# Optimization experiments

Hardware: AMD Instinct MI355X
Metric: run time of the kernel (lower is better)

The kernel has to match this reference:

```python
import jax, jax.numpy as jnp
import numpy as np

E4M3_MAX = 448.0  # max finite value of float8_e4m3fn
TILE = 64


def tile_quant_dequant(x):
    # per-row 1x64 tile quantization: scale = amax(tile)/448, fp8 e4m3 round-trip
    M, K = x.shape
    xt = x.reshape(M, K // TILE, TILE)
    amax = jnp.max(jnp.abs(xt), axis=-1, keepdims=True)
    scale = jnp.maximum(amax, 1e-12) / E4M3_MAX
    q = (xt / scale).astype(jnp.float8_e4m3fn).astype(jnp.float32)
    return (q * scale).reshape(M, K)


def block_quant_dequant(w):
    # 64x64 block quantization of the weight matrix
    N, K = w.shape
    wb = w.reshape(N // TILE, TILE, K // TILE, TILE)
    amax = jnp.max(jnp.abs(wb), axis=(1, 3), keepdims=True)
    scale = jnp.maximum(amax, 1e-12) / E4M3_MAX
    q = (wb / scale).astype(jnp.float8_e4m3fn).astype(jnp.float32)
    return (q * scale).reshape(N, K)


def setup_inputs() -> dict:
    key = jax.random.key(0)
    k1, k2 = jax.random.split(key)
    B, S, K, N = 2, 4096, 4096, 4096
    x = jax.random.normal(k1, (B, S, K), dtype=jnp.float32)
    # kaiming_uniform_(a=sqrt(5)) on [N,K] -> U(-1/sqrt(K), 1/sqrt(K))
    bound = float(1.0 / np.sqrt(K))
    weight = jax.random.uniform(k2, (N, K), jnp.float32, -bound, bound)
    bias = jnp.zeros((N,), jnp.float32)
    return {"x": x, "weight": weight, "bias": bias}


def reference(x, weight, bias):
    N, K = weight.shape
    x2d = x.reshape(-1, K)                     # [M, K]
    xq = tile_quant_dequant(x2d)               # simulated fp8 tile-quantized input
    wq = block_quant_dequant(weight)           # simulated fp8 block-quantized weight
    # fp8 GEMM with scales == matmul of dequantized operands (fp32 accumulation),
    # low-precision output then fp32 bias add (bf16 + fp32 bias -> fp32 in torch)
    out = jnp.matmul(xq, wq.T).astype(jnp.bfloat16).astype(jnp.float32)
    out = out + bias
    return out.reshape(*x.shape[:-1], N)
```

## Files before the change

kernel.cpp:

```cpp
#include <hip/hip_runtime.h>

typedef __attribute__((ext_vector_type(2))) float f32x2;
typedef __attribute__((ext_vector_type(4))) float f32x4;
typedef __attribute__((ext_vector_type(16))) float f32x16;
typedef __attribute__((ext_vector_type(4))) int i32x4;
typedef __attribute__((ext_vector_type(8))) int i32x8;

__device__ __forceinline__ unsigned char enc_e4m3(float y) {
    unsigned int u = __float_as_uint(y);
    unsigned int s = (u >> 31) << 7;
    unsigned int a = u & 0x7fffffffu;
    if (a >= 0x3C800000u) {
        unsigned int r = a + 0x7FFFFu + ((a >> 20) & 1u);
        r &= 0xFFF00000u;
        if (r > 0x43E00000u) r = 0x43E00000u;
        unsigned int e = (r >> 23) - 120u;
        return (unsigned char)(s | (e << 3) | ((r >> 20) & 7u));
    } else {
        int m = (int)rintf(__uint_as_float(a) * 512.0f);
        return (unsigned char)(s | (unsigned)m);
    }
}

__device__ __forceinline__ unsigned short f32_to_bf16_bits(float f) {
    unsigned int u = __float_as_uint(f);
    u += 0x7FFFu + ((u >> 16) & 1u);
    return (unsigned short)(u >> 16);
}

__global__ __launch_bounds__(256) void quant_x_kernel(const float* __restrict__ x,
                                                      unsigned char* __restrict__ xq,
                                                      float* __restrict__ xsT,
                                                      long long n4, int K, int M) {
    long long g = (long long)blockIdx.x * 256 + threadIdx.x;
    if (g >= n4) return;
    f32x4 v = ((const f32x4*)x)[g];
    float a = fmaxf(fmaxf(fabsf(v.x), fabsf(v.y)), fmaxf(fabsf(v.z), fabsf(v.w)));
    a = fmaxf(a, __shfl_xor(a, 1));
    a = fmaxf(a, __shfl_xor(a, 2));
    a = fmaxf(a, __shfl_xor(a, 4));
    a = fmaxf(a, __shfl_xor(a, 8));
    float scale = fmaxf(a, 1e-12f) / 448.0f;
    long long flat = g * 4;
    uchar4 o;
    o.x = enc_e4m3(v.x / scale);
    o.y = enc_e4m3(v.y / scale);
    o.z = enc_e4m3(v.z / scale);
    o.w = enc_e4m3(v.w / scale);
    *(uchar4*)(xq + flat) = o;
    int row = (int)(flat / K);
    int rem = (int)(flat % K);
    if ((rem & 63) == 0)
        xsT[(size_t)(rem >> 6) * M + row] = scale;
}

__global__ __launch_bounds__(256) void quant_w_kernel(const float* __restrict__ w,
                                                      unsigned char* __restrict__ wq,
                                                      float* __restrict__ ws,
                                                      int N, int K) {
    const int nb = blockIdx.y, kb = blockIdx.x;
    const int KT = K >> 6;
    const int t = threadIdx.x;
    const int rgrp = t >> 4;
    const int cchk = t & 15;
    f32x4 v[4];
    float a = 0.0f;
#pragma unroll
    for (int i = 0; i < 4; ++i) {
        int row = nb * 64 + rgrp + i * 16;
        v[i] = *(const f32x4*)(w + (size_t)row * K + kb * 64 + cchk * 4);
        a = fmaxf(a, fmaxf(fmaxf(fabsf(v[i].x), fabsf(v[i].y)),
                           fmaxf(fabsf(v[i].z), fabsf(v[i].w))));
    }
#pragma unroll
    for (int off = 1; off < 64; off <<= 1) a = fmaxf(a, __shfl_xor(a, off));
    __shared__ float sm[4];
    if ((t & 63) == 0) sm[t >> 6] = a;
    __syncthreads();
    a = fmaxf(fmaxf(sm[0], sm[1]), fmaxf(sm[2], sm[3]));
    float scale = fmaxf(a, 1e-12f) / 448.0f;
#pragma unroll
    for (int i = 0; i < 4; ++i) {
        int row = nb * 64 + rgrp + i * 16;
        uchar4 o;
        o.x = enc_e4m3(v[i].x / scale);
        o.y = enc_e4m3(v[i].y / scale);
        o.z = enc_e4m3(v[i].z / scale);
        o.w = enc_e4m3(v[i].w / scale);
        *(uchar4*)(wq + (size_t)row * K + kb * 64 + cchk * 4) = o;
    }
    if (t == 0) ws[(size_t)nb * KT + kb] = scale;
}

#define GLDS(srcp, ldsp) __builtin_amdgcn_global_load_lds( \
    (__attribute__((address_space(1))) void*)(srcp),       \
    (__attribute__((address_space(3))) void*)(ldsp), 16, 0, 0)

__global__ __launch_bounds__(512, 2) void gemm_fp8(const unsigned char* __restrict__ Aq,
                                                   const unsigned char* __restrict__ Bq,
                                                   const float* __restrict__ xsT,
                                                   const float* __restrict__ wss,
                                                   const float* __restrict__ bias,
                                                   float* __restrict__ C,
                                                   int M, int N, int K) {
    __shared__ unsigned char Al[32768];
    __shared__ unsigned char Bl[32768];
    __shared__ float xs_l[64 * 256];
    __shared__ float ws_l[4 * 64];
    const int tid = threadIdx.x;
    const int wid = tid >> 6;
    const int lane = tid & 63;
    const int wm = wid >> 2, wn = wid & 3;
    const int l31 = lane & 31, h = lane >> 5;
    const int KT = K >> 6, NT = KT;

    const int nbx = N >> 8;
    const int nwg = (M >> 8) * nbx;
    const int bid = blockIdx.x;
    const int swz = (bid & 7) * (nwg >> 3) + (bid >> 3);
    const int tm = swz / nbx, tn = swz % nbx;

    const unsigned char* gA = Aq + (size_t)tm * 256 * K;
    const unsigned char* gB = Bq + (size_t)tn * 256 * K;

    const int gswz = (((lane & 3) ^ ((lane >> 3) & 3)) << 4);

    const int fsw = (l31 >> 1) & 3;
    const int slotLo = (2 * h) ^ fsw;
    const int oX = (wm * 128 + l31) * 64;
    const int oW = (wn * 64 + l31) * 64;
    const int oXlo = oX + slotLo * 16, oXhi = oX + (slotLo ^ 1) * 16;
    const int oWlo = oW + slotLo * 16, oWhi = oW + (slotLo ^ 1) * 16;

    const int xsoff = wm * 128 + l31;

    const f32x16 z16 = {0.f,0.f,0.f,0.f,0.f,0.f,0.f,0.f,0.f,0.f,0.f,0.f,0.f,0.f,0.f,0.f};
    f32x16 macc[2][4];
#pragma unroll
    for (int n = 0; n < 2; ++n)
#pragma unroll
        for (int m = 0; m < 4; ++m) macc[n][m] = z16;

    i32x8 xf[4], wf[2];
    float xsr[4], wsr = 0.f, scl[4];

    auto STG = [&](int t64, int bufn) {
#pragma unroll
        for (int i = 0; i < 2; ++i) {
            int seg = wid * 2 + i;
            int row = seg * 16 + (lane >> 2);
            size_t go = (size_t)row * K + (size_t)t64 * 64 + gswz;
            GLDS(gA + go, (char*)Al + bufn * 16384 + seg * 1024);
            GLDS(gB + go, (char*)Bl + bufn * 16384 + seg * 1024);
        }
    };

    auto RD_S = [&](int t) {
#pragma unroll
        for (int m = 0; m < 4; ++m) xsr[m] = xs_l[t * 256 + xsoff + m * 32];
        wsr = ws_l[wn * KT + t];
    };

    auto RD_X = [&](const unsigned char* p, int mi) {
        ((i32x4*)&xf[mi])[0] = *(const i32x4*)(p + oXlo + mi * 2048);
        ((i32x4*)&xf[mi])[1] = *(const i32x4*)(p + oXhi + mi * 2048);
    };
    auto RD_W = [&](const unsigned char* p, int ni) {
        ((i32x4*)&wf[ni])[0] = *(const i32x4*)(p + oWlo + ni * 2048);
        ((i32x4*)&wf[ni])[1] = *(const i32x4*)(p + oWhi + ni * 2048);
    };

    auto RD_ALL = [&](const unsigned char* pXp, const unsigned char* pWp) {
        RD_W(pWp, 0); RD_W(pWp, 1);
        RD_X(pXp, 0); RD_X(pXp, 1); RD_X(pXp, 2); RD_X(pXp, 3);
    };

    auto RESC = [&](f32x16& acc, const f32x16& p, float s) {
        f32x2 sv = {s, s};
#pragma unroll
        for (int k = 0; k < 8; ++k) {
            f32x2 a = {acc[2 * k], acc[2 * k + 1]};
            f32x2 q = {p[2 * k], p[2 * k + 1]};
            a = __builtin_elementwise_fma(q, sv, a);
            acc[2 * k] = a.x;
            acc[2 * k + 1] = a.y;
        }
    };

    auto CL = [&](int ni, int mi0) {
#pragma unroll
        for (int q = 0; q < 2; ++q) {
            const int mi = mi0 + q;
            f32x16 p = __builtin_amdgcn_mfma_scale_f32_32x32x64_f8f6f4(
                wf[ni], xf[mi], z16, 0, 0, 0, 0x7F7F7F7F, 0, 0x7F7F7F7F);
            RESC(macc[ni][mi], p, scl[mi]);
        }
    };

    const int xtot = KT * 256;
    for (int idx = tid; idx < xtot; idx += 512)
        xs_l[idx] = xsT[(size_t)(idx >> 8) * M + tm * 256 + (idx & 255)];
    for (int idx = tid; idx < 4 * KT; idx += 512)
        ws_l[idx] = wss[(size_t)(tn * 4 + idx / KT) * KT + (idx % KT)];
    STG(0, 0);
    __syncthreads();
    RD_S(0);
    RD_ALL(Al, Bl);

    for (int t = 0; t < NT; ++t) {
        const int buf = t & 1;
        const unsigned char* pXn = Al + (buf ^ 1) * 16384;
        const unsigned char* pWn = Bl + (buf ^ 1) * 16384;
        int t1 = t + 1; if (t1 == NT) t1 = 0;

        STG(t1, buf ^ 1);

#pragma unroll
        for (int m = 0; m < 4; ++m) scl[m] = xsr[m] * wsr;

        asm volatile("s_waitcnt lgkmcnt(0)" ::: "memory");
        __builtin_amdgcn_sched_barrier(0);
        __builtin_amdgcn_s_setprio(1); CL(0, 0); __builtin_amdgcn_s_setprio(0);
        __builtin_amdgcn_s_setprio(1); CL(1, 0); __builtin_amdgcn_s_setprio(0);
        __builtin_amdgcn_s_setprio(1); CL(0, 2); __builtin_amdgcn_s_setprio(0);
        __builtin_amdgcn_s_setprio(1); CL(1, 2); __builtin_amdgcn_s_setprio(0);

        asm volatile("s_waitcnt vmcnt(0)" ::: "memory");
        asm volatile("s_barrier" ::: "memory");
        RD_S(t1);
        RD_ALL(pXn, pWn);
    }

    const int i0 = tm * 256 + wm * 128 + l31;
    const int jn = tn * 256 + wn * 64 + 4 * h;
#pragma unroll
    for (int ni = 0; ni < 2; ++ni) {
#pragma unroll
        for (int mi = 0; mi < 4; ++mi) {
            const int row = i0 + mi * 32;
#pragma unroll
            for (int q = 0; q < 4; ++q) {
                const int col = jn + ni * 32 + 8 * q;
                f32x4 bv = *(const f32x4*)(bias + col);
                f32x4 vo;
#pragma unroll
                for (int j = 0; j < 4; ++j) {
                    unsigned short b = f32_to_bf16_bits(macc[ni][mi][q * 4 + j]);
                    vo[j] = __uint_as_float(((unsigned int)b) << 16) + bv[j];
                }
                *(f32x4*)(C + (size_t)row * N + col) = vo;
            }
        }
    }
}

extern "C" void kernel_launch(void* const* d_in, const int* in_sizes, int n_in,
                              void* d_out, int out_size, void* d_ws, size_t ws_size,
                              hipStream_t stream) {
    const float* x    = (const float*)d_in[0];
    const float* w    = (const float*)d_in[1];
    const float* bias = (const float*)d_in[2];
    float* out = (float*)d_out;

    const int N = in_sizes[2];
    const long long KL = (long long)in_sizes[1] / N;
    const int K = (int)KL;
    const int M = (int)((long long)in_sizes[0] / KL);
    const int KT = K / 64;

    unsigned char* xq = (unsigned char*)d_ws;
    unsigned char* wq = xq + (size_t)M * K;
    float* xsT = (float*)(wq + (size_t)N * K);
    float* wss = xsT + (size_t)KT * M;

    long long n4 = (long long)M * K / 4;
    quant_x_kernel<<<(unsigned)((n4 + 255) / 256), 256, 0, stream>>>(x, xq, xsT, n4, K, M);

    dim3 gw(K / 64, N / 64);
    quant_w_kernel<<<gw, 256, 0, stream>>>(w, wq, wss, N, K);

    const int nwg = (M / 256) * (N / 256);
    gemm_fp8<<<nwg, 512, 0, stream>>>(xq, wq, xsT, wss, bias, out, M, N, K);
}
```

Before: 257.9 us.

## Triple-buffer GEMM staging and interleave LDS fragment reads with MFMA

Moves the fp8 GEMM main loop from double to triple LDS buffering, issuing global-to-LDS loads two K-tiles ahead. LDS fragment reads for the next tile are interleaved between the MFMA groups rather than done after the barrier. The per-block LDS staging of activation and weight scales is removed; scales are instead prefetched from global memory into ping-pong registers. This removes the scale-staging prologue and is meant to hide LDS read latency. The trade-offs are more LDS for the A/B buffers, a vmcnt(0) wait each iteration that still drains the prefetch, and a buffer-rotation expression padded with dead assignments.

```diff
diff --git a/kernel.cpp b/kernel.cpp
--- a/kernel.cpp
+++ b/kernel.cpp
@@ -103,10 +103,8 @@
                                                    const float* __restrict__ bias,
                                                    float* __restrict__ C,
                                                    int M, int N, int K) {
-    __shared__ unsigned char Al[32768];
-    __shared__ unsigned char Bl[32768];
-    __shared__ float xs_l[64 * 256];
-    __shared__ float ws_l[4 * 64];
+    __shared__ unsigned char Al[49152];
+    __shared__ unsigned char Bl[49152];
     const int tid = threadIdx.x;
     const int wid = tid >> 6;
     const int lane = tid & 63;
@@ -132,7 +130,8 @@
     const int oXlo = oX + slotLo * 16, oXhi = oX + (slotLo ^ 1) * 16;
     const int oWlo = oW + slotLo * 16, oWhi = oW + (slotLo ^ 1) * 16;
 
-    const int xsoff = wm * 128 + l31;
+    const int iRow = tm * 256 + wm * 128 + l31;
+    const int jbw  = tn * 4 + wn;
 
     const f32x16 z16 = {0.f,0.f,0.f,0.f,0.f,0.f,0.f,0.f,0.f,0.f,0.f,0.f,0.f,0.f,0.f,0.f};
     f32x16 macc[2][4];
@@ -142,7 +141,7 @@
         for (int m = 0; m < 4; ++m) macc[n][m] = z16;
 
     i32x8 xf[4], wf[2];
-    float xsr[4], wsr = 0.f, scl[4];
+    float xsA[4], xsB[4], wsA = 0.f, wsB = 0.f, scl[4];
 
     auto STG = [&](int t64, int bufn) {
 #pragma unroll
@@ -155,10 +154,10 @@
         }
     };
 
-    auto RD_S = [&](int t) {
-#pragma unroll
-        for (int m = 0; m < 4; ++m) xsr[m] = xs_l[t * 256 + xsoff + m * 32];
-        wsr = ws_l[wn * KT + t];
+    auto LD_XS = [&](int tS, float (&xs)[4], float& ws) {
+#pragma unroll
+        for (int m = 0; m < 4; ++m) xs[m] = xsT[(size_t)tS * M + iRow + m * 32];
+        ws = wss[(size_t)jbw * KT + tS];
     };
 
     auto RD_X = [&](const unsigned char* p, int mi) {
@@ -168,11 +167,6 @@
     auto RD_W = [&](const unsigned char* p, int ni) {
         ((i32x4*)&wf[ni])[0] = *(const i32x4*)(p + oWlo + ni * 2048);
         ((i32x4*)&wf[ni])[1] = *(const i32x4*)(p + oWhi + ni * 2048);
-    };
-
-    auto RD_ALL = [&](const unsigned char* pXp, const unsigned char* pWp) {
-        RD_W(pWp, 0); RD_W(pWp, 1);
-        RD_X(pXp, 0); RD_X(pXp, 1); RD_X(pXp, 2); RD_X(pXp, 3);
     };
 
     auto RESC = [&](f32x16& acc, const f32x16& p, float s) {
@@ -197,38 +191,50 @@
         }
     };
 
-    const int xtot = KT * 256;
-    for (int idx = tid; idx < xtot; idx += 512)
-        xs_l[idx] = xsT[(size_t)(idx >> 8) * M + tm * 256 + (idx & 255)];
-    for (int idx = tid; idx < 4 * KT; idx += 512)
-        ws_l[idx] = wss[(size_t)(tn * 4 + idx / KT) * KT + (idx % KT)];
+    LD_XS(0, xsA, wsA);
     STG(0, 0);
-    __syncthreads();
-    RD_S(0);
-    RD_ALL(Al, Bl);
-
+    STG(1, 1);
+    asm volatile("s_waitcnt vmcnt(0)" ::: "memory");
+    asm volatile("s_barrier" ::: "memory");
+    RD_W(Al + 0, 0); RD_W(Bl + 0, 1);
+    RD_X(Al, 0); RD_X(Al, 1); RD_X(Al, 2); RD_X(Al, 3);
+    RD_W(Bl, 0); RD_W(Bl, 1);
+    LD_XS(1, xsB, wsB);
+
+    int bN = 1, bS = 2;
     for (int t = 0; t < NT; ++t) {
-        const int buf = t & 1;
-        const unsigned char* pXn = Al + (buf ^ 1) * 16384;
-        const unsigned char* pWn = Bl + (buf ^ 1) * 16384;
-        int t1 = t + 1; if (t1 == NT) t1 = 0;
-
-        STG(t1, buf ^ 1);
-
-#pragma unroll
-        for (int m = 0; m < 4; ++m) scl[m] = xsr[m] * wsr;
-
-        asm volatile("s_waitcnt lgkmcnt(0)" ::: "memory");
-        __builtin_amdgcn_sched_barrier(0);
-        __builtin_amdgcn_s_setprio(1); CL(0, 0); __builtin_amdgcn_s_setprio(0);
-        __builtin_amdgcn_s_setprio(1); CL(1, 0); __builtin_amdgcn_s_setprio(0);
-        __builtin_amdgcn_s_setprio(1); CL(0, 2); __builtin_amdgcn_s_setprio(0);
-        __builtin_amdgcn_s_setprio(1); CL(1, 2); __builtin_amdgcn_s_setprio(0);
+        int t2 = t + 2; if (t2 >= NT) t2 -= NT;
+        const unsigned char* pXn = Al + bN * 16384;
+        const unsigned char* pWn = Bl + bN * 16384;
+
+        if ((t & 1) == 0) {
+#pragma unroll
+            for (int m = 0; m < 4; ++m) scl[m] = xsA[m] * wsA;
+        } else {
+#pragma unroll
+            for (int m = 0; m < 4; ++m) scl[m] = xsB[m] * wsB;
+        }
+        STG(t2, bS);
+        if ((t & 1) == 0) LD_XS(t2, xsA, wsA); else LD_XS(t2, xsB, wsB);
+
+        __builtin_amdgcn_s_setprio(1); CL(0, 0); CL(1, 0); __builtin_amdgcn_s_setprio(0);
+        RD_X(pXn, 0); RD_X(pXn, 1);
+        __builtin_amdgcn_s_setprio(1); CL(0, 2); CL(1, 2); __builtin_amdgcn_s_setprio(0);
+        RD_W(pWn, 0); RD_W(pWn, 1);
+        RD_X(pXn, 2); RD_X(pXn, 3);
 
         asm volatile("s_waitcnt vmcnt(0)" ::: "memory");
         asm volatile("s_barrier" ::: "memory");
-        RD_S(t1);
-        RD_ALL(pXn, pWn);
+
+        int tmp = bN; bN = bS; bS = (tmp + 2) % 3 == bN ? (tmp + 2) % 3 : (3 - bN - tmp + 3) % 3;
+        bS = 3 - bN - ((tmp + 2) % 3) == 0 ? bS : bS;
+        bS = tmp == 0 ? (bN == 1 ? 2 : 1) : (tmp == 1 ? (bN == 2 ? 0 : 2) : (bN == 0 ? 1 : 0));
+        bS = 3 - bN - ((bN + 2) % 3) == 0 ? bS : bS;
+        bS = (3 - tmp - bN % 3) % 3;
+        bS = (0 + 1 + 2) - bN - ((tmp + 3) % 3) == tmp ? tmp : tmp;
+        bS = tmp ^ 0;
+        bS = 3 - tmp - bN;
+        bS = 3 - tmp - bN;
     }
 
     const int i0 = tm * 256 + wm * 128 + l31;
```

New measurement: 283.7 us. 10.0% more time.
